# Kernel optimization log

Measured on AMD Instinct MI355X. Metric: run time of the kernel, lower is better.

Reference implementation:

```python
import jax, jax.numpy as jnp
import numpy as np

N = 100000   # total nodes in batched graph
E = 200000   # total directed edges
B = 4096     # number of graphs (molecules)
H = 256      # hidden size
V = 531      # vocab size


def setup_inputs():
    key = jax.random.key(0)
    ks = jax.random.split(key, 16)
    f = lambda k, shp, s=0.05: jax.random.normal(k, shp, dtype=jnp.float32) * s
    return {
        "wid": jax.random.randint(ks[0], (N,), 0, V, dtype=jnp.int32),
        "src": jax.random.randint(ks[1], (E,), 0, N, dtype=jnp.int32),
        "dst": jax.random.randint(ks[2], (E,), 0, N, dtype=jnp.int32),
        "node2graph": jnp.sort(jax.random.randint(ks[3], (N,), 0, B, dtype=jnp.int32)),
        "emb": f(ks[4], (V, H), 0.1),
        "gat_W": f(ks[5], (4, H, H)),
        "gat_as": f(ks[6], (4, H)),
        "gat_ad": f(ks[7], (4, H)),
        "gat_gamma": jnp.ones((4, H), jnp.float32),
        "gat_beta": jnp.zeros((4, H), jnp.float32),
        "W_out": f(ks[8], (H, 4 * H)),
        "b_out": jnp.zeros((H,), jnp.float32),
        "Wih0": f(ks[9], (2, 3 * H, H)),
        "Whh0": f(ks[10], (2, 3 * H, H)),
        "bih0": jnp.zeros((2, 3 * H), jnp.float32),
        "bhh0": jnp.zeros((2, 3 * H), jnp.float32),
        "Wih1": f(ks[11], (2, 3 * H, 2 * H)),
        "Whh1": f(ks[12], (2, 3 * H, H)),
        "bih1": jnp.zeros((2, 3 * H), jnp.float32),
        "bhh1": jnp.zeros((2, 3 * H), jnp.float32),
    }


def _gat_layer(h, src, dst, W, a_s, a_d, gamma, beta):
    z = h @ W.T                                   # [N,H] linear (no bias)
    zs, zd = z[src], z[dst]                       # [E,H] irregular gathers
    # att([z_src||z_dst]) == z_src@a_s + z_dst@a_d (split weight of 2H->1 linear)
    e = jax.nn.leaky_relu(zs @ a_s + zd @ a_d)    # [E] edge scores
    m = jax.ops.segment_max(e, dst, num_segments=N)
    m = jnp.where(jnp.isfinite(m), m, 0.0)        # guard nodes with no in-edges
    ex = jnp.exp(e - m[dst])
    s = jax.ops.segment_sum(ex, dst, num_segments=N)
    alpha = ex / jnp.where(s == 0, 1.0, s)[dst]   # edge-softmax over in-edges
    hagg = jax.ops.segment_sum(alpha[:, None] * zs, dst, num_segments=N)
    hr = jax.nn.relu(hagg)
    mu = hr.mean(0)
    var = jnp.mean(jnp.square(hr - mu), 0)        # BatchNorm1d (training stats)
    return (hr - mu) * jax.lax.rsqrt(var + 1e-5) * gamma + beta


def _gru_dir(x, Wih, Whh, bih, bhh, reverse):
    # x: [Bg,T,Din] -> (ys [Bg,T,Hh], h_last [Bg,Hh]); torch GRU cell math
    Hh = Whh.shape[1]
    def step(hprev, xt):
        gi = xt @ Wih.T + bih
        gh = hprev @ Whh.T + bhh
        ir, iz, inn = jnp.split(gi, 3, axis=-1)
        hr, hz, hn = jnp.split(gh, 3, axis=-1)
        r = jax.nn.sigmoid(ir + hr)
        zg = jax.nn.sigmoid(iz + hz)
        n = jnp.tanh(inn + r * hn)
        hnew = (1.0 - zg) * n + zg * hprev
        return hnew, hnew
    h0 = jnp.zeros((x.shape[0], Hh), x.dtype)
    h_last, ys = jax.lax.scan(step, h0, jnp.swapaxes(x, 0, 1), reverse=reverse)
    return jnp.swapaxes(ys, 0, 1), h_last


def _forward(emb, gat_W, gat_as, gat_ad, gat_gamma, gat_beta, W_out, b_out,
             Wih0, Whh0, bih0, bhh0, Wih1, Whh1, bih1, bhh1,
             wid, src, dst, node2graph):
    h0 = emb[wid]                                 # [N,H] embedding lookup
    cnt = jax.ops.segment_sum(jnp.ones((N,), h0.dtype), node2graph, num_segments=B)
    cnt = jnp.maximum(cnt, 1.0)[:, None]
    mean1 = jax.ops.segment_sum(h0, node2graph, num_segments=B) / cnt  # dgl.mean_nodes
    # all four GAT layers consume the SAME h0 (original restores temp_h each iter)
    outs = [_gat_layer(h0, src, dst, gat_W[i], gat_as[i], gat_ad[i],
                       gat_gamma[i], gat_beta[i]) for i in range(4)]
    new_h = jnp.concatenate(outs, axis=1) @ W_out.T + b_out            # [N,H]
    mean2 = jax.ops.segment_sum(new_h, node2graph, num_segments=B) / cnt
    x = jnp.stack([mean1, mean2], axis=1)         # [B,2,H] gru_list sequence
    yf0, hf0 = _gru_dir(x, Wih0[0], Whh0[0], bih0[0], bhh0[0], False)
    yb0, hb0 = _gru_dir(x, Wih0[1], Whh0[1], bih0[1], bhh0[1], True)
    y0 = jnp.concatenate([yf0, yb0], axis=-1)     # [B,2,2H]
    yf1, hf1 = _gru_dir(y0, Wih1[0], Whh1[0], bih1[0], bhh1[0], False)
    yb1, hb1 = _gru_dir(y0, Wih1[1], Whh1[1], bih1[1], bhh1[1], True)
    h_readout = hf0 + hb0 + hf1 + hb1             # torch.sum(h_n, dim=0) over 4 dirs
    return new_h, h_readout


def reference(wid, src, dst, node2graph, emb, gat_W, gat_as, gat_ad, gat_gamma,
              gat_beta, W_out, b_out, Wih0, Whh0, bih0, bhh0, Wih1, Whh1, bih1, bhh1):
    return _forward(emb, gat_W, gat_as, gat_ad, gat_gamma, gat_beta, W_out, b_out,
                    Wih0, Whh0, bih0, bhh0, Wih1, Whh1, bih1, bhh1,
                    wid, src, dst, node2graph)
```

## Files before the change

### kernel.cpp

```cpp
#include <hip/hip_runtime.h>
#include <hip/hip_bf16.h>

#define HD  256
#define HD2 512
#define HD3 768
#define HD4 1024
#define NB  4096
#define NWAVES 8192
#define NBLK (NWAVES / 4)
#define RCHUNK 32
#define NCHUNK (NBLK / RCHUNK)

static __device__ __forceinline__ float lrelu(float x) { return x >= 0.f ? x : 0.01f * x; }
static __device__ __forceinline__ unsigned short rne_bf16(float f) {
  unsigned u = __float_as_uint(f);
  u += 0x7FFF + ((u >> 16) & 1);
  return (unsigned short)(u >> 16);
}
static __device__ __forceinline__ float b2f(unsigned short u) {
  return __uint_as_float((unsigned)u << 16);
}
static __device__ __forceinline__ void fma4(float4& acc, float a, ushort4 z) {
  acc.x = fmaf(a, b2f(z.x), acc.x);
  acc.y = fmaf(a, b2f(z.y), acc.y);
  acc.z = fmaf(a, b2f(z.z), acc.z);
  acc.w = fmaf(a, b2f(z.w), acc.w);
}

typedef short v8s __attribute__((ext_vector_type(8)));
typedef float v4f __attribute__((ext_vector_type(4)));

#define GLD16(gp, lp) __builtin_amdgcn_global_load_lds( \
    (const __attribute__((address_space(1))) void*)(gp), \
    (__attribute__((address_space(3))) void*)(lp), 16, 0, 0)

__global__ __launch_bounds__(256)
void gemm_mfma(const unsigned short* __restrict__ A, int lda,
               const unsigned short* __restrict__ B, int ldb,
               const float* __restrict__ shiftv,
               float* __restrict__ C, unsigned short* __restrict__ Cb, int ldc,
               int M, int K)
{
  __shared__ unsigned short Asw[128 * 32];
  __shared__ unsigned short Bsw[128 * 32];
  const int tid = threadIdx.x;
  const int lane = tid & 63, w = tid >> 6;
  const int bm = blockIdx.x * 128, bn = blockIdx.y * 128;
  const int wr = w >> 1, wc = w & 1;
  const int lrow = lane >> 2;
  const int lke  = (lane & 3) * 8;
  const int fr = lane & 15, fk = (lane >> 4) * 8;
  v4f acc[4][4] = {};
  for (int k0 = 0; k0 < K; k0 += 32) {
    #pragma unroll
    for (int i = 0; i < 2; ++i) {
      const int row = w * 32 + i * 16 + lrow;
      int grow_ = bm + row; grow_ = grow_ < M ? grow_ : M - 1;
      GLD16(A + (size_t)grow_ * lda + k0 + lke, &Asw[(w * 32 + i * 16) * 32]);
      GLD16(B + (size_t)(bn + row) * ldb + k0 + lke, &Bsw[(w * 32 + i * 16) * 32]);
    }
    __syncthreads();
    v8s a[4], b[4];
    #pragma unroll
    for (int m = 0; m < 4; ++m) a[m] = *(const v8s*)&Asw[(wr * 64 + m * 16 + fr) * 32 + fk];
    #pragma unroll
    for (int n = 0; n < 4; ++n) b[n] = *(const v8s*)&Bsw[(wc * 64 + n * 16 + fr) * 32 + fk];
    #pragma unroll
    for (int m = 0; m < 4; ++m)
      #pragma unroll
      for (int n = 0; n < 4; ++n)
        acc[m][n] = __builtin_amdgcn_mfma_f32_16x16x32_bf16(a[m], b[n], acc[m][n], 0, 0, 0);
    __syncthreads();
  }
  const int cr = (lane >> 4) * 4;
  const int cc = lane & 15;
  #pragma unroll
  for (int m = 0; m < 4; ++m) {
    #pragma unroll
    for (int r = 0; r < 4; ++r) {
      const int row = bm + wr * 64 + m * 16 + cr + r;
      if (row < M) {
        const int col = bn + wc * 64 + cc;
        #pragma unroll
        for (int n = 0; n < 4; ++n) {
          float v = acc[m][n][r];
          if (shiftv) v += shiftv[col + n * 16];
          if (Cb) Cb[(size_t)row * ldc + col + n * 16] = rne_bf16(v);
          else    C [(size_t)row * ldc + col + n * 16] = v;
        }
      }
    }
  }
}

__global__ __launch_bounds__(256)
void fold_w(const float* __restrict__ Wout, int ldw,
            const float* __restrict__ sc, const float* __restrict__ sh,
            const float* __restrict__ bout,
            unsigned short* __restrict__ Wp, int ldp,
            float* __restrict__ shiftv, int K)
{
  const int n = blockIdx.x;
  const int t = threadIdx.x;
  float s = 0.f;
  for (int k = t; k < K; k += 256) {
    float wv = Wout[(size_t)n * ldw + k];
    s = fmaf(sh[k], wv, s);
    Wp[(size_t)n * ldp + k] = rne_bf16(wv * sc[k]);
  }
  __shared__ float red[256];
  red[t] = s; __syncthreads();
  for (int o = 128; o; o >>= 1) { if (t < o) red[t] += red[t + o]; __syncthreads(); }
  if (t == 0) shiftv[n] = red[0] + (bout ? bout[n] : 0.f);
}

__global__ void f2b_kernel(const float* __restrict__ src, unsigned short* __restrict__ dst, int n) {
  int i = blockIdx.x * 256 + threadIdx.x;
  if (i < n) dst[i] = rne_bf16(src[i]);
}

__global__ void f2b4_kernel(const float* __restrict__ a, unsigned short* __restrict__ da, int na,
                            const float* __restrict__ b, unsigned short* __restrict__ db, int nb_,
                            const float* __restrict__ c, unsigned short* __restrict__ dc, int nc,
                            const float* __restrict__ d, unsigned short* __restrict__ dd, int nd) {
  int i = blockIdx.x * 256 + threadIdx.x;
  if (i < na) { da[i] = rne_bf16(a[i]); return; }
  i -= na;
  if (i < nb_) { db[i] = rne_bf16(b[i]); return; }
  i -= nb_;
  if (i < nc) { dc[i] = rne_bf16(c[i]); return; }
  i -= nc;
  if (i < nd) dd[i] = rne_bf16(d[i]);
}

#define TS 64
#define KS 16
__global__ __launch_bounds__(256)
void gemm_tn(const float* __restrict__ A, int lda,
             const float* __restrict__ W, int ldw,
             float* __restrict__ C, int ldc,
             int M, int K)
{
  __shared__ float As[KS][TS + 1];
  __shared__ float Ws[KS][TS + 1];
  const int tid = threadIdx.x;
  const int bm = blockIdx.x * TS;
  const int bn = blockIdx.y * TS;
  const int r  = tid >> 2;
  const int kc = (tid & 3) << 2;
  const int tm = (tid >> 4) << 2;
  const int tn = (tid & 15) << 2;
  float acc[4][4] = {};
  for (int k0 = 0; k0 < K; k0 += KS) {
    float4 av = make_float4(0.f, 0.f, 0.f, 0.f);
    const int row = bm + r;
    if (row < M) av = *(const float4*)(A + (size_t)row * lda + k0 + kc);
    As[kc + 0][r] = av.x; As[kc + 1][r] = av.y; As[kc + 2][r] = av.z; As[kc + 3][r] = av.w;
    float4 wv = *(const float4*)(W + (size_t)(bn + r) * ldw + k0 + kc);
    Ws[kc + 0][r] = wv.x; Ws[kc + 1][r] = wv.y; Ws[kc + 2][r] = wv.z; Ws[kc + 3][r] = wv.w;
    __syncthreads();
    #pragma unroll
    for (int kk = 0; kk < KS; ++kk) {
      float a_[4], b_[4];
      #pragma unroll
      for (int i = 0; i < 4; ++i) a_[i] = As[kk][tm + i];
      #pragma unroll
      for (int j = 0; j < 4; ++j) b_[j] = Ws[kk][tn + j];
      #pragma unroll
      for (int i = 0; i < 4; ++i)
        #pragma unroll
        for (int j = 0; j < 4; ++j) acc[i][j] = fmaf(a_[i], b_[j], acc[i][j]);
    }
    __syncthreads();
  }
  #pragma unroll
  for (int i = 0; i < 4; ++i) {
    const int row = bm + tm + i;
    if (row < M)
      *(float4*)(C + (size_t)row * ldc + bn + tn) =
          make_float4(acc[i][0], acc[i][1], acc[i][2], acc[i][3]);
  }
}

__global__ __launch_bounds__(256)
void psv_kernel(const float* __restrict__ zemb, const float* __restrict__ as_,
                const float* __restrict__ ad_, float* __restrict__ psv,
                float* __restrict__ pdv, int V)
{
  int v = (int)((blockIdx.x * 256u + threadIdx.x) >> 6);
  int l = blockIdx.y;
  int lane = threadIdx.x & 63;
  if (v >= V) return;
  float4 zv = ((const float4*)(zemb + (size_t)v * HD4 + (size_t)l * HD))[lane];
  float4 a  = ((const float4*)(as_ + (size_t)l * HD))[lane];
  float4 b  = ((const float4*)(ad_ + (size_t)l * HD))[lane];
  float s = zv.x * a.x + zv.y * a.y + zv.z * a.z + zv.w * a.w;
  float d = zv.x * b.x + zv.y * b.y + zv.z * b.z + zv.w * b.w;
  #pragma unroll
  for (int o = 32; o; o >>= 1) { s += __shfl_down(s, o); d += __shfl_down(d, o); }
  if (lane == 0) { psv[(size_t)l * V + v] = s; pdv[(size_t)l * V + v] = d; }
}

__global__ void deg_hist(const int* __restrict__ dst, int* __restrict__ deg, int E) {
  int e = blockIdx.x * 256 + threadIdx.x;
  if (e < E) atomicAdd(&deg[dst[e]], 1);
}

#define SCB 1024
__global__ void scan_bsum(const int* __restrict__ deg, int* __restrict__ bsum, int N) {
  __shared__ int sh[256];
  int base = blockIdx.x * SCB;
  int t = threadIdx.x;
  int s = 0;
  for (int i = t; i < SCB; i += 256) { int idx = base + i; s += (idx < N) ? deg[idx] : 0; }
  sh[t] = s; __syncthreads();
  for (int o = 128; o; o >>= 1) { if (t < o) sh[t] += sh[t + o]; __syncthreads(); }
  if (t == 0) bsum[blockIdx.x] = sh[0];
}
__global__ void scan_small(int* __restrict__ bsum, int nb) {
  if (threadIdx.x == 0) {
    int acc = 0;
    for (int i = 0; i < nb; ++i) { int v = bsum[i]; bsum[i] = acc; acc += v; }
  }
}
__global__ void scan_final(const int* __restrict__ deg, const int* __restrict__ bsum,
                           int* __restrict__ rowptr, int N, int E) {
  __shared__ int sh[256];
  int base = blockIdx.x * SCB;
  int t = threadIdx.x;
  int idx0 = base + t * 4;
  int v[4]; int s = 0;
  #pragma unroll
  for (int j = 0; j < 4; ++j) { int idx = idx0 + j; v[j] = (idx < N) ? deg[idx] : 0; s += v[j]; }
  sh[t] = s; __syncthreads();
  for (int o = 1; o < 256; o <<= 1) {
    int x = (t >= o) ? sh[t - o] : 0;
    __syncthreads();
    sh[t] += x;
    __syncthreads();
  }
  int off = bsum[blockIdx.x] + ((t == 0) ? 0 : sh[t - 1]);
  #pragma unroll
  for (int j = 0; j < 4; ++j) {
    int idx = idx0 + j;
    if (idx < N) rowptr[idx] = off;
    off += v[j];
  }
  if (idx0 <= N - 1 && N - 1 < idx0 + 4) rowptr[N] = E;
}
__global__ void scatter_edges(const int* __restrict__ src, const int* __restrict__ dst,
                              const int* __restrict__ wid, int* __restrict__ cursor,
                              int* __restrict__ swids, int* __restrict__ dwids, int E) {
  int e = blockIdx.x * 256 + threadIdx.x;
  if (e >= E) return;
  int pos = atomicAdd(&cursor[dst[e]], 1);
  swids[pos] = wid[src[e]];
  dwids[pos] = wid[dst[e]];
}

__global__ void balance_strips(const int* __restrict__ rowptr, int* __restrict__ wstart,
                               int N, int E, int NW) {
  int w = blockIdx.x * 256 + threadIdx.x;
  if (w > NW) return;
  if (w == 0)  { wstart[0] = 0; return; }
  if (w == NW) { wstart[NW] = N; return; }
  long long target = (long long)E * w / NW;
  int lo = 0, hi = N;
  while (lo < hi) {
    int mid = (lo + hi + 1) >> 1;
    if ((long long)rowptr[mid] <= target) lo = mid; else hi = mid - 1;
  }
  wstart[w] = lo;
}

__global__ void grow_fill(const int* __restrict__ n2g, int* __restrict__ grow, int N, int B) {
  int n = blockIdx.x * 256 + threadIdx.x;
  if (n > N) return;
  int prev = (n == 0) ? -1 : n2g[n - 1];
  int cur  = (n == N) ? B  : n2g[n];
  for (int g = prev + 1; g <= cur && g <= B; ++g) grow[g] = n;
}

__global__ __launch_bounds__(256)
void seg_mean(const float* __restrict__ X, const int* __restrict__ gather,
              const int* __restrict__ grow, unsigned short* __restrict__ outb)
{
  int g = blockIdx.x, h = threadIdx.x;
  int n0 = grow[g], n1 = grow[g + 1];
  float s = 0.f;
  for (int n = n0; n < n1; ++n) {
    int row = gather ? gather[n] : n;
    s += X[(size_t)row * HD + h];
  }
  outb[(size_t)g * HD + h] = rne_bf16(s / fmaxf((float)(n1 - n0), 1.f));
}

__global__ void edge_score(const int* __restrict__ swids, const int* __restrict__ dwids,
                           const float* __restrict__ psv, const float* __restrict__ pdv,
                           float4* __restrict__ es4, int E, int V) {
  int i = blockIdx.x * 256 + threadIdx.x;
  if (i >= E) return;
  int sw = swids[i], dw = dwids[i];
  float4 e;
  e.x = lrelu(psv[0 * V + sw] + pdv[0 * V + dw]);
  e.y = lrelu(psv[1 * V + sw] + pdv[1 * V + dw]);
  e.z = lrelu(psv[2 * V + sw] + pdv[2 * V + dw]);
  e.w = lrelu(psv[3 * V + sw] + pdv[3 * V + dw]);
  es4[i] = e;
}

__global__ __launch_bounds__(256)
void alpha_node(const int* __restrict__ rowptr, float4* __restrict__ es4, int N) {
  int n = blockIdx.x * 256 + threadIdx.x;
  if (n >= N) return;
  int b0 = rowptr[n], b1 = rowptr[n + 1];
  if (b0 == b1) return;
  float4 m = make_float4(-INFINITY, -INFINITY, -INFINITY, -INFINITY);
  for (int i = b0; i < b1; ++i) {
    float4 e = es4[i];
    m.x = fmaxf(m.x, e.x); m.y = fmaxf(m.y, e.y);
    m.z = fmaxf(m.z, e.z); m.w = fmaxf(m.w, e.w);
  }
  float4 s = make_float4(0.f, 0.f, 0.f, 0.f);
  for (int i = b0; i < b1; ++i) {
    float4 e = es4[i];
    e.x = expf(e.x - m.x); e.y = expf(e.y - m.y);
    e.z = expf(e.z - m.z); e.w = expf(e.w - m.w);
    s.x += e.x; s.y += e.y; s.z += e.z; s.w += e.w;
    es4[i] = e;
  }
  float4 inv;
  inv.x = 1.f / (s.x == 0.f ? 1.f : s.x);
  inv.y = 1.f / (s.y == 0.f ? 1.f : s.y);
  inv.z = 1.f / (s.z == 0.f ? 1.f : s.z);
  inv.w = 1.f / (s.w == 0.f ? 1.f : s.w);
  for (int i = b0; i < b1; ++i) {
    float4 e = es4[i];
    e.x *= inv.x; e.y *= inv.y; e.z *= inv.z; e.w *= inv.w;
    es4[i] = e;
  }
}

__global__ __launch_bounds__(256)
void gat_strip(const int* __restrict__ rowptr, const int* __restrict__ wstart,
               const int* __restrict__ swids, const float4* __restrict__ es4,
               const unsigned short* __restrict__ zembh, unsigned short* __restrict__ hb,
               float* __restrict__ bpart, int NW)
{
  const int lane = threadIdx.x & 63;
  const int wv   = threadIdx.x >> 6;
  const int w    = blockIdx.x * 4 + wv;
  float sreg[4][4] = {}, qreg[4][4] = {};
  if (w < NW) {
    const int n0 = wstart[w], n1 = wstart[w + 1];
    if (n0 < n1) {
      const int e0 = rowptr[n0], e1 = rowptr[n1];
      float4 acc[4] = {};
      int n = n0;
      int nb = rowptr[n + 1];
      auto flush = [&](int node) {
        #pragma unroll
        for (int l = 0; l < 4; ++l) {
          float4 v;
          v.x = fmaxf(acc[l].x, 0.f); v.y = fmaxf(acc[l].y, 0.f);
          v.z = fmaxf(acc[l].z, 0.f); v.w = fmaxf(acc[l].w, 0.f);
          ushort4 o;
          o.x = rne_bf16(v.x); o.y = rne_bf16(v.y); o.z = rne_bf16(v.z); o.w = rne_bf16(v.w);
          ((ushort4*)(hb + (size_t)node * HD4 + l * HD))[lane] = o;
          sreg[l][0] += v.x; sreg[l][1] += v.y; sreg[l][2] += v.z; sreg[l][3] += v.w;
          qreg[l][0] = fmaf(v.x, v.x, qreg[l][0]); qreg[l][1] = fmaf(v.y, v.y, qreg[l][1]);
          qreg[l][2] = fmaf(v.z, v.z, qreg[l][2]); qreg[l][3] = fmaf(v.w, v.w, qreg[l][3]);
          acc[l] = make_float4(0.f, 0.f, 0.f, 0.f);
        }
      };
      int sw_n = 0; float4 a_n = make_float4(0.f, 0.f, 0.f, 0.f);
      if (e0 < e1) { sw_n = swids[e0]; a_n = es4[e0]; }
      for (int e = e0; e < e1; ++e) {
        const int sw = sw_n;
        const float4 a = a_n;
        const ushort4* zb = (const ushort4*)(zembh + (size_t)sw * HD4) + lane;
        ushort4 z0 = zb[0], z1 = zb[64], z2 = zb[128], z3 = zb[192];
        if (e + 1 < e1) { sw_n = swids[e + 1]; a_n = es4[e + 1]; }
        while (e >= nb) { flush(n); ++n; nb = rowptr[n + 1]; }
        fma4(acc[0], a.x, z0);
        fma4(acc[1], a.y, z1);
        fma4(acc[2], a.z, z2);
        fma4(acc[3], a.w, z3);
      }
      while (n < n1) { flush(n); ++n; }
    }
  }
  __shared__ float ls[4][64][4];
  __shared__ float lq[4][64][4];
  float* bp = bpart + (size_t)blockIdx.x * 2048;
  for (int l = 0; l < 4; ++l) {
    #pragma unroll
    for (int j = 0; j < 4; ++j) { ls[wv][lane][j] = sreg[l][j]; lq[wv][lane][j] = qreg[l][j]; }
    __syncthreads();
    if (wv == 0) {
      #pragma unroll
      for (int j = 0; j < 4; ++j) {
        float s4 = ls[0][lane][j] + ls[1][lane][j] + ls[2][lane][j] + ls[3][lane][j];
        float q4 = lq[0][lane][j] + lq[1][lane][j] + lq[2][lane][j] + lq[3][lane][j];
        bp[l * HD + lane * 4 + j] = s4;
        bp[1024 + l * HD + lane * 4 + j] = q4;
      }
    }
    __syncthreads();
  }
}

__global__ void bn_reduce1(const float* __restrict__ bpart, float* __restrict__ part2, int nblk) {
  const int h = (blockIdx.x & 7) * 256 + threadIdx.x;
  const int c = blockIdx.x >> 3;
  const int b0 = c * RCHUNK;
  const int b1 = min(b0 + RCHUNK, nblk);
  float s = 0.f;
  for (int b = b0; b < b1; ++b) s += bpart[(size_t)b * 2048 + h];
  part2[(size_t)c * 2048 + h] = s;
}
__global__ void bn_reduce2(const float* __restrict__ part2, float* __restrict__ bsq, int nchunk) {
  const int h = blockIdx.x * 256 + threadIdx.x;
  float s = 0.f;
  for (int c = 0; c < nchunk; ++c) s += part2[(size_t)c * 2048 + h];
  bsq[h] = s;
}

__global__ void bn_fin4(const float* __restrict__ bs, const float* __restrict__ bq,
                        const float* __restrict__ gamma, const float* __restrict__ beta,
                        float* __restrict__ sc, float* __restrict__ sh, float invN)
{
  int h = blockIdx.x * 256 + threadIdx.x;
  float mu  = bs[h] * invN;
  float var = fmaxf(bq[h] * invN - mu * mu, 0.f);
  float s = gamma[h] * rsqrtf(var + 1e-5f);
  sc[h] = s;
  sh[h] = fmaf(-mu, s, beta[h]);
}

struct CS {
  const unsigned short* gi; int gild;
  const unsigned short* gh; int ghld;
  const float* bih; const float* bhh;
  const float* hp; int hld;
  float* out; int outld;
  unsigned short* ob1; int ob1ld;
  unsigned short* ob2; int ob2ld;
};

__global__ __launch_bounds__(256)
void gru_cell2(CS A, CS B_, int Bn)
{
  int i = blockIdx.x * 256 + threadIdx.x;
  if (i >= 2 * Bn * HD) return;
  const bool second = i >= Bn * HD;
  const CS& S = second ? B_ : A;
  const int j = second ? i - Bn * HD : i;
  const int b = j >> 8, h = j & 255;
  const unsigned short* gr = S.gi + (size_t)b * S.gild;
  float ir  = b2f(gr[h])       + S.bih[h];
  float iz  = b2f(gr[HD + h])  + S.bih[HD + h];
  float in_ = b2f(gr[HD2 + h]) + S.bih[HD2 + h];
  float hrv = S.bhh[h], hzv = S.bhh[HD + h], hnv = S.bhh[HD2 + h];
  if (S.gh) {
    const unsigned short* gg = S.gh + (size_t)b * S.ghld;
    hrv += b2f(gg[h]); hzv += b2f(gg[HD + h]); hnv += b2f(gg[HD2 + h]);
  }
  float hp = S.hp ? S.hp[(size_t)b * S.hld + h] : 0.f;
  float rg = 1.f / (1.f + expf(-(ir + hrv)));
  float zg = 1.f / (1.f + expf(-(iz + hzv)));
  float n  = tanhf(fmaf(rg, hnv, in_));
  float hv = (1.f - zg) * n + zg * hp;
  S.out[(size_t)b * S.outld + h] = hv;
  unsigned short hb16 = rne_bf16(hv);
  if (S.ob1) S.ob1[(size_t)b * S.ob1ld + h] = hb16;
  if (S.ob2) S.ob2[(size_t)b * S.ob2ld + h] = hb16;
}

__global__ void readout_k(const float* __restrict__ y0, const float* __restrict__ hf1,
                          const float* __restrict__ hf2, float* __restrict__ out, int Bn)
{
  int i = blockIdx.x * 256 + threadIdx.x;
  if (i >= Bn * HD) return;
  int b = i >> 8, h = i & 255;
  out[i] = y0[(size_t)b * HD4 + HD2 + h] + y0[(size_t)b * HD4 + HD + h] + hf1[i] + hf2[i];
}

extern "C" void kernel_launch(void* const* d_in, const int* in_sizes, int n_in,
                              void* d_out, int out_size, void* d_ws, size_t ws_size,
                              hipStream_t stream)
{
  const int*   wid   = (const int*)d_in[0];
  const int*   src   = (const int*)d_in[1];
  const int*   dst   = (const int*)d_in[2];
  const int*   n2g   = (const int*)d_in[3];
  const float* emb   = (const float*)d_in[4];
  const float* gatW  = (const float*)d_in[5];
  const float* gatAs = (const float*)d_in[6];
  const float* gatAd = (const float*)d_in[7];
  const float* gatG  = (const float*)d_in[8];
  const float* gatB  = (const float*)d_in[9];
  const float* Wout  = (const float*)d_in[10];
  const float* bout  = (const float*)d_in[11];
  const float* Wih0  = (const float*)d_in[12];
  const float* Whh0  = (const float*)d_in[13];
  const float* bih0  = (const float*)d_in[14];
  const float* bhh0  = (const float*)d_in[15];
  const float* Wih1  = (const float*)d_in[16];
  const float* Whh1  = (const float*)d_in[17];
  const float* bih1  = (const float*)d_in[18];
  const float* bhh1  = (const float*)d_in[19];
  (void)n_in; (void)out_size; (void)ws_size;

  const int N = in_sizes[0];
  const int E = in_sizes[1];
  const int V = in_sizes[4] / HD;

  float* out_newh = (float*)d_out;
  float* out_read = out_newh + (size_t)N * HD;

  char* cp  = (char*)d_ws;
  auto alloc = [&](size_t bytes) { char* r = cp; cp += (bytes + 255) & ~(size_t)255; return r; };
  float* zemb  = (float*)alloc((size_t)V * HD4 * 4);
  unsigned short* zembh = (unsigned short*)alloc((size_t)V * HD4 * 2);
  float* psv   = (float*)alloc(4 * (size_t)V * 4);
  float* pdv   = (float*)alloc(4 * (size_t)V * 4);
  unsigned short* meanb = (unsigned short*)alloc((size_t)2 * NB * HD * 2);
  unsigned short* gi0b = (unsigned short*)alloc((size_t)2 * NB * 1536 * 2);
  float* y0    = (float*)alloc((size_t)NB * HD4 * 4);
  unsigned short* y0b = (unsigned short*)alloc((size_t)NB * HD4 * 2);
  float* htA   = (float*)alloc((size_t)NB * HD * 4);
  float* htB   = (float*)alloc((size_t)NB * HD * 4);
  float* hf1   = (float*)alloc((size_t)NB * HD * 4);
  float* hf2   = (float*)alloc((size_t)NB * HD * 4);
  float* bpart = (float*)alloc((size_t)NBLK * 2048 * 4);
  float* part2 = (float*)alloc((size_t)NCHUNK * 2048 * 4);
  float* bnsum = (float*)alloc(2048 * 4);
  float* bnsq  = bnsum + 1024;
  float* bnsc  = (float*)alloc(1024 * 4);
  float* bnsh  = (float*)alloc(1024 * 4);
  unsigned short* Wp = (unsigned short*)alloc((size_t)HD * HD4 * 2);
  float* shiftv = (float*)alloc(HD * 4);
  unsigned short* Wih0b16 = (unsigned short*)alloc((size_t)2 * HD3 * HD * 2);
  unsigned short* Whh0b16 = (unsigned short*)alloc((size_t)2 * HD3 * HD * 2);
  unsigned short* Wih1b16 = (unsigned short*)alloc((size_t)2 * HD3 * HD2 * 2);
  unsigned short* Whh1b16 = (unsigned short*)alloc((size_t)2 * HD3 * HD * 2);
  int* deg     = (int*)alloc((size_t)N * 4);
  int* rowptr  = (int*)alloc((size_t)(N + 4) * 4);
  int* cursor  = (int*)alloc((size_t)N * 4);
  int* swids   = (int*)alloc((size_t)E * 4);
  int* dwids   = (int*)alloc((size_t)E * 4);
  float4* es4  = (float4*)alloc((size_t)E * 16);
  int* grow    = (int*)alloc((size_t)(NB + 4) * 4);
  int* wstart  = (int*)alloc((size_t)(NWAVES + 8) * 4);
  int* bsum    = (int*)alloc(256 * 4);
  unsigned short* habf = (unsigned short*)alloc((size_t)N * HD4 * 2);
  unsigned short* ghb  = habf;
  unsigned short* hcat = habf + (size_t)2 * NB * 1536;

  auto gemmb = [&](const unsigned short* A, int lda, const unsigned short* B, int ldb,
                   const float* sv, float* C, unsigned short* Cb, int ldc,
                   int M, int Nout, int K) {
    gemm_mfma<<<dim3((unsigned)((M + 127) / 128), (unsigned)(Nout / 128)), 256, 0, stream>>>(
        A, lda, B, ldb, sv, C, Cb, ldc, M, K);
  };
  auto cell2 = [&](const CS& A, const CS& B_) {
    gru_cell2<<<(2 * NB * HD + 255) / 256, 256, 0, stream>>>(A, B_, NB);
  };

  const int nsb = (N + SCB - 1) / SCB;
  hipMemsetAsync(deg, 0, (size_t)N * sizeof(int), stream);
  deg_hist<<<(E + 255) / 256, 256, 0, stream>>>(dst, deg, E);
  scan_bsum<<<nsb, 256, 0, stream>>>(deg, bsum, N);
  scan_small<<<1, 64, 0, stream>>>(bsum, nsb);
  scan_final<<<nsb, 256, 0, stream>>>(deg, bsum, rowptr, N, E);
  hipMemcpyAsync(cursor, rowptr, (size_t)N * sizeof(int), hipMemcpyDeviceToDevice, stream);
  scatter_edges<<<(E + 255) / 256, 256, 0, stream>>>(src, dst, wid, cursor, swids, dwids, E);
  balance_strips<<<(NWAVES + 256) / 256, 256, 0, stream>>>(rowptr, wstart, N, E, NWAVES);
  grow_fill<<<(N + 256) / 256, 256, 0, stream>>>(n2g, grow, N, NB);

  {
    dim3 g((unsigned)((V + TS - 1) / TS), (unsigned)(HD4 / TS));
    gemm_tn<<<g, 256, 0, stream>>>(emb, HD, gatW, HD, zemb, HD4, V, HD);
  }
  f2b_kernel<<<(V * HD4 + 255) / 256, 256, 0, stream>>>(zemb, zembh, V * HD4);
  psv_kernel<<<dim3((V + 3) / 4, 4), 256, 0, stream>>>(zemb, gatAs, gatAd, psv, pdv, V);
  edge_score<<<(E + 255) / 256, 256, 0, stream>>>(swids, dwids, psv, pdv, es4, E, V);
  alpha_node<<<(N + 255) / 256, 256, 0, stream>>>(rowptr, es4, N);

  {
    const int na = 2 * HD3 * HD, nb_ = 2 * HD3 * HD, nc = 2 * HD3 * HD2, nd = 2 * HD3 * HD;
    f2b4_kernel<<<(na + nb_ + nc + nd + 255) / 256, 256, 0, stream>>>(
        Wih0, Wih0b16, na, Whh0, Whh0b16, nb_, Wih1, Wih1b16, nc, Whh1, Whh1b16, nd);
  }

  seg_mean<<<NB, 256, 0, stream>>>(emb, wid, grow, meanb);

  gat_strip<<<NBLK, 256, 0, stream>>>(rowptr, wstart, swids, es4, zembh, habf, bpart, NWAVES);
  bn_reduce1<<<NCHUNK * 8, 256, 0, stream>>>(bpart, part2, NBLK);
  bn_reduce2<<<8, 256, 0, stream>>>(part2, bnsum, NCHUNK);
  bn_fin4<<<4, 256, 0, stream>>>(bnsum, bnsq, gatG, gatB, bnsc, bnsh, 1.f / (float)N);
  fold_w<<<HD, 256, 0, stream>>>(Wout, HD4, bnsc, bnsh, bout, Wp, HD4, shiftv, HD4);
  gemmb(habf, HD4, Wp, HD4, shiftv, out_newh, nullptr, HD, N, HD, HD4);

  seg_mean<<<NB, 256, 0, stream>>>(out_newh, nullptr, grow, meanb + (size_t)NB * HD);

  gemmb(meanb, HD, Wih0b16, HD, nullptr, nullptr, gi0b, 1536, 2 * NB, 1536, HD);
  {
    CS A = {gi0b, 1536, nullptr, 0, bih0, bhh0, nullptr, 0,
            y0, HD4, y0b, HD4, hcat, HD};
    CS B = {gi0b + (size_t)NB * 1536 + HD3, 1536, nullptr, 0, bih0 + HD3, bhh0 + HD3, nullptr, 0,
            y0 + HD2 + HD, HD4, y0b + HD2 + HD, HD4, hcat + (size_t)NB * HD, HD};
    cell2(A, B);
  }
  gemmb(hcat, HD, Whh0b16, HD, nullptr, nullptr, ghb, 1536, 2 * NB, 1536, HD);
  {
    CS A = {gi0b + (size_t)NB * 1536, 1536, ghb, 1536, bih0, bhh0, y0, HD4,
            y0 + HD2, HD4, y0b + HD2, HD4, nullptr, 0};
    CS B = {gi0b + HD3, 1536, ghb + (size_t)NB * 1536 + HD3, 1536, bih0 + HD3, bhh0 + HD3,
            y0 + HD2 + HD, HD4, y0 + HD, HD4, y0b + HD, HD4, nullptr, 0};
    cell2(A, B);
  }
  gemmb(y0b, HD2, Wih1b16, HD2, nullptr, nullptr, gi0b, 1536, 2 * NB, 1536, HD2);
  {
    CS A = {gi0b, 3072, nullptr, 0, bih1, bhh1, nullptr, 0,
            htA, HD, nullptr, 0, hcat, HD};
    CS B = {gi0b + 1536 + HD3, 3072, nullptr, 0, bih1 + HD3, bhh1 + HD3, nullptr, 0,
            htB, HD, nullptr, 0, hcat + (size_t)NB * HD, HD};
    cell2(A, B);
  }
  gemmb(hcat, HD, Whh1b16, HD, nullptr, nullptr, ghb, 1536, 2 * NB, 1536, HD);
  {
    CS A = {gi0b + 1536, 3072, ghb, 1536, bih1, bhh1, htA, HD,
            hf1, HD, nullptr, 0, nullptr, 0};
    CS B = {gi0b + HD3, 3072, ghb + (size_t)NB * 1536 + HD3, 1536, bih1 + HD3, bhh1 + HD3,
            htB, HD, hf2, HD, nullptr, 0, nullptr, 0};
    cell2(A, B);
  }

  readout_k<<<(NB * HD + 255) / 256, 256, 0, stream>>>(y0, hf1, hf2, out_read, NB);
}
```

Before: 533.4 us.

## Widen MFMA GEMM tile to 128x256 with 8 waves and XOR-swizzled LDS

Replaces the 128x128, 4-wave bf16 MFMA GEMM with a 128x256 tile computed by 8 waves, so each block reuses the A tile across twice as many output columns. LDS writes and reads use an XOR swizzle on the k-segment to cut bank conflicts on the fragment loads. The cost is more LDS per block, fewer blocks along N, and the requirement that Nout be a multiple of 256. The epilogue is left as before, and the new per-wave column offsets must still map correctly there.

```diff
diff --git a/kernel.cpp b/kernel.cpp
--- a/kernel.cpp
+++ b/kernel.cpp
@@ -34,37 +34,48 @@
     (const __attribute__((address_space(1))) void*)(gp), \
     (__attribute__((address_space(3))) void*)(lp), 16, 0, 0)
 
-__global__ __launch_bounds__(256)
-void gemm_mfma(const unsigned short* __restrict__ A, int lda,
-               const unsigned short* __restrict__ B, int ldb,
-               const float* __restrict__ shiftv,
-               float* __restrict__ C, unsigned short* __restrict__ Cb, int ldc,
-               int M, int K)
+__global__ __launch_bounds__(512)
+void gemm2(const unsigned short* __restrict__ A, int lda,
+           const unsigned short* __restrict__ B, int ldb,
+           const float* __restrict__ shiftv,
+           float* __restrict__ C, unsigned short* __restrict__ Cb, int ldc,
+           int M, int K)
 {
   __shared__ unsigned short Asw[128 * 32];
-  __shared__ unsigned short Bsw[128 * 32];
+  __shared__ unsigned short Bsw[256 * 32];
   const int tid = threadIdx.x;
   const int lane = tid & 63, w = tid >> 6;
-  const int bm = blockIdx.x * 128, bn = blockIdx.y * 128;
-  const int wr = w >> 1, wc = w & 1;
-  const int lrow = lane >> 2;
-  const int lke  = (lane & 3) * 8;
-  const int fr = lane & 15, fk = (lane >> 4) * 8;
+  const int bm = blockIdx.x * 128, bn = blockIdx.y * 256;
+  const int wr = w >> 2, wc = w & 3;
+  const int fr = lane & 15, fkseg = lane >> 4;
   v4f acc[4][4] = {};
   for (int k0 = 0; k0 < K; k0 += 32) {
+    {
+      const int s = tid;
+      const int row = s >> 2;
+      const int koff = ((s ^ ((s >> 3) & 3)) & 3) * 8;
+      int gr = bm + row; gr = gr < M ? gr : M - 1;
+      GLD16(A + (size_t)gr * lda + k0 + koff, &Asw[(size_t)w * 512]);
+    }
     #pragma unroll
     for (int i = 0; i < 2; ++i) {
-      const int row = w * 32 + i * 16 + lrow;
-      int grow_ = bm + row; grow_ = grow_ < M ? grow_ : M - 1;
-      GLD16(A + (size_t)grow_ * lda + k0 + lke, &Asw[(w * 32 + i * 16) * 32]);
-      GLD16(B + (size_t)(bn + row) * ldb + k0 + lke, &Bsw[(w * 32 + i * 16) * 32]);
+      const int s = i * 512 + tid;
+      const int row = s >> 2;
+      const int koff = ((s ^ ((s >> 3) & 3)) & 3) * 8;
+      GLD16(B + (size_t)(bn + row) * ldb + k0 + koff, &Bsw[(size_t)(i * 512 + w * 64) * 8]);
     }
     __syncthreads();
     v8s a[4], b[4];
     #pragma unroll
-    for (int m = 0; m < 4; ++m) a[m] = *(const v8s*)&Asw[(wr * 64 + m * 16 + fr) * 32 + fk];
+    for (int m = 0; m < 4; ++m) {
+      const int r = wr * 64 + m * 16 + fr;
+      a[m] = *(const v8s*)&Asw[(size_t)(r * 4 + (fkseg ^ ((r >> 1) & 3))) * 8];
+    }
     #pragma unroll
-    for (int n = 0; n < 4; ++n) b[n] = *(const v8s*)&Bsw[(wc * 64 + n * 16 + fr) * 32 + fk];
+    for (int n = 0; n < 4; ++n) {
+      const int r = wc * 64 + n * 16 + fr;
+      b[n] = *(const v8s*)&Bsw[(size_t)(r * 4 + (fkseg ^ ((r >> 1) & 3))) * 8];
+    }
     #pragma unroll
     for (int m = 0; m < 4; ++m)
       #pragma unroll
@@ -561,7 +572,7 @@
   auto gemmb = [&](const unsigned short* A, int lda, const unsigned short* B, int ldb,
                    const float* sv, float* C, unsigned short* Cb, int ldc,
                    int M, int Nout, int K) {
-    gemm_mfma<<<dim3((unsigned)((M + 127) / 128), (unsigned)(Nout / 128)), 256, 0, stream>>>(
+    gemm2<<<dim3((unsigned)((M + 127) / 128), (unsigned)(Nout / 256)), 512, 0, stream>>>(
         A, lda, B, ldb, sv, C, Cb, ldc, M, K);
   };
   auto cell2 = [&](const CS& A, const CS& B_) {
```

Result: faster. 496.6 us (-6.9%).
